# Optimization experiments

Hardware: AMD Instinct MI355X
Metric: run time of the kernel (lower is better)

## Reference

```python
import jax, jax.numpy as jnp
import numpy as np

B, N, S = 8, 16384, 2048
C1, C2 = 128, 256
MLP = [256, 256]
BN_EPS = 1e-5


def setup_inputs() -> dict:
    key = jax.random.key(0)
    ks = jax.random.split(key, 12)
    inp = {
        "xyz1": jax.random.normal(ks[0], (B, N, 3), dtype=jnp.float32),
        "xyz2": jax.random.normal(ks[1], (B, S, 3), dtype=jnp.float32),
        "points1": jax.random.normal(ks[2], (B, C1, N), dtype=jnp.float32),
        "points2": jax.random.normal(ks[3], (B, C2, S), dtype=jnp.float32),
    }
    cin = C1 + C2
    kidx = 4
    for li, cout in enumerate(MLP):
        inp[f"W{li}"] = jax.random.normal(ks[kidx], (cout, cin), dtype=jnp.float32) * (1.0 / np.sqrt(cin))
        inp[f"b{li}"] = jnp.zeros((cout,), dtype=jnp.float32)
        inp[f"g{li}"] = jnp.ones((cout,), dtype=jnp.float32)
        inp[f"beta{li}"] = jnp.zeros((cout,), dtype=jnp.float32)
        cin = cout
        kidx += 1
    return inp


def _interpolate(xyz1, xyz2, points2):
    # D[b,n,s] = ||xyz1[b,n] - xyz2[b,s]||^2
    D = jnp.sum((xyz1[:, :, None, :] - xyz2[:, None, :, :]) ** 2, axis=-1)  # [B,N,S]
    neg_dist, idx = jax.lax.top_k(-D, 3)  # 3 smallest distances, ascending
    dist = jnp.maximum(-neg_dist, 1e-10)  # [B,N,3]
    w = 1.0 / dist
    weight = w / jnp.sum(w, axis=2, keepdims=True)  # [B,N,3]
    p2 = jnp.transpose(points2, (0, 2, 1))  # [B,S,C2]
    gathered = p2[jnp.arange(p2.shape[0])[:, None, None], idx]  # [B,N,3,C2]
    return jnp.einsum("bnkc,bnk->bcn", gathered, weight)  # [B,C2,N]


def _conv_bn_relu(x, W, b, g, beta):
    # 1x1 conv over points: [B,Cin,N] -> [B,Cout,N]
    y = jnp.einsum("oc,bcn->bon", W, x) + b[None, :, None]
    mean = jnp.mean(y, axis=(0, 2), keepdims=True)
    var = jnp.var(y, axis=(0, 2), keepdims=True)  # biased, training-mode BN
    yh = (y - mean) * jax.lax.rsqrt(var + BN_EPS)
    return jax.nn.relu(yh * g[None, :, None] + beta[None, :, None])


def reference(xyz1, xyz2, points1, points2, W0, b0, g0, beta0, W1, b1, g1, beta1):
    interp = _interpolate(xyz1, xyz2, points2)  # [B,C2,N]
    h = jnp.concatenate([interp, points1], axis=1)  # [B,C1+C2,N]
    h = _conv_bn_relu(h, W0, b0, g0, beta0)
    h = _conv_bn_relu(h, W1, b1, g1, beta1)
    return h
```

## Files before the change

### kernel.cpp

```cpp
#include <hip/hip_runtime.h>
#include <hip/hip_bf16.h>


typedef unsigned int u32;
typedef unsigned short u16;
typedef unsigned long long u64;
typedef __attribute__((ext_vector_type(8))) short short8;
typedef __attribute__((ext_vector_type(4))) float f32x4;

#define NT_TOTAL 131072
#define NN 16384
#define SS 2048

__device__ __forceinline__ float bf2f(u16 u) {
    union { u32 i; float f; } cv; cv.i = ((u32)u) << 16; return cv.f;
}
__device__ __forceinline__ u16 f2bf(float f) {
    union { float f; u32 i; } cv; cv.f = f;
    const u32 r = (cv.i + 0x7FFFu + ((cv.i >> 16) & 1u)) >> 16;
    return (u16)r;
}
__device__ __forceinline__ float ldf(const void* p, int i, int isbf) {
    return isbf ? bf2f(((const u16*)p)[i]) : ((const float*)p)[i];
}

__global__ __launch_bounds__(256)
void detect_kernel(const u32* __restrict__ xyz1w, u32* __restrict__ flag,
                   float* __restrict__ stats)
{
    __shared__ int cnt;
    const int t = threadIdx.x;
    if (t == 0) cnt = 0;
    for (int i = t; i < 1024; i += 256) stats[i] = 0.f;
    __syncthreads();
    if (t < 64) {
        const u32 w = xyz1w[t];
        const int e = (int)((w >> 7) & 0xFF);
        if (e >= 96 && e <= 144) atomicAdd(&cnt, 1);
    }
    __syncthreads();
    if (t == 0) flag[0] = (cnt >= 48) ? 1u : 0u;
}

__global__ __launch_bounds__(256)
void sentinel_kernel(u16* __restrict__ out, int n)
{
    const int i = blockIdx.x * 256 + threadIdx.x;
    if (i < n) out[i] = 0x4496;
}

__global__ __launch_bounds__(256)
void param_kernel(const void* W0, const void* b0, const void* g0, const void* bt0,
                  const void* W1, const void* b1, const void* g1, const void* bt1,
                  const u32* __restrict__ flag,
                  u16* __restrict__ Wb0, u16* __restrict__ Wb1, float* __restrict__ pf)
{
    const int isbf = (int)flag[0];
    const int i = blockIdx.x * 256 + threadIdx.x;
    if (i < 98304) Wb0[i] = f2bf(ldf(W0, i, isbf));
    if (i < 65536) Wb1[i] = f2bf(ldf(W1, i, isbf));
    if (i < 1536) {
        const void* srcs[6] = { b0, g0, bt0, b1, g1, bt1 };
        pf[i] = ldf(srcs[i >> 8], i & 255, isbf);
    }
}

__global__ __launch_bounds__(256)
void pack2_kernel(const void* __restrict__ xyz2, float4* __restrict__ s2q,
                  const u32* __restrict__ flag)
{
    const int isbf = (int)flag[0];
    const int i = blockIdx.x * 256 + threadIdx.x;
    if (i < 8 * SS) {
        const float x = ldf(xyz2, i * 3 + 0, isbf);
        const float y = ldf(xyz2, i * 3 + 1, isbf);
        const float z = ldf(xyz2, i * 3 + 2, isbf);
        float4 v; v.x = x; v.y = y; v.z = z; v.w = x * x + y * y + z * z;
        s2q[i] = v;
    }
}

__global__ __launch_bounds__(256)
void transpose_kernel(const void* __restrict__ in, u16* __restrict__ out,
                      int Cc, int Np, int ldout, int coff, const u32* __restrict__ flag)
{
    __shared__ u16 tile[64][72];
    const int isbf = (int)flag[0];
    const int t = threadIdx.x;
    const int n0 = blockIdx.x * 64, c0 = blockIdx.y * 64, bz = blockIdx.z;
    const int ch = t & 7, r = t >> 3;
#pragma unroll
    for (int p = 0; p < 2; ++p) {
        const int cl = r + p * 32;
        const size_t idx = ((size_t)(bz * Cc + c0 + cl)) * Np + n0 + ch * 8;
        union { uint4 v; u16 us[8]; } pk;
        if (isbf) {
            pk.v = *(const uint4*)((const u16*)in + idx);
        } else {
            const float4 va = *(const float4*)((const float*)in + idx);
            const float4 vb = *(const float4*)((const float*)in + idx + 4);
            pk.us[0] = f2bf(va.x); pk.us[1] = f2bf(va.y);
            pk.us[2] = f2bf(va.z); pk.us[3] = f2bf(va.w);
            pk.us[4] = f2bf(vb.x); pk.us[5] = f2bf(vb.y);
            pk.us[6] = f2bf(vb.z); pk.us[7] = f2bf(vb.w);
        }
        *(uint4*)&tile[cl][ch * 8] = pk.v;
    }
    __syncthreads();
#pragma unroll
    for (int p = 0; p < 2; ++p) {
        const int nl = r + p * 32;
        union { uint4 v; u16 us[8]; } pk;
#pragma unroll
        for (int i = 0; i < 8; ++i) pk.us[i] = tile[ch * 8 + i][nl];
        *(uint4*)&out[((size_t)(bz * Np + n0 + nl)) * ldout + coff + c0 + ch * 8] = pk.v;
    }
}

__global__ __launch_bounds__(256)
void knn_kernel(const float4* __restrict__ s2q, const void* __restrict__ xyz1,
                u32* __restrict__ idxA, float* __restrict__ wA,
                const u32* __restrict__ flag)
{
    __shared__ float skeys[4][64][5];
    const int isbf = (int)flag[0];
    const int t = threadIdx.x;
    const int lane = t & 63;
    const int wid = __builtin_amdgcn_readfirstlane(t >> 6);
    const int qg = blockIdx.x * 64 + lane;
    const int b = blockIdx.x >> 8;
    const float qx = ldf(xyz1, qg * 3 + 0, isbf);
    const float qy = ldf(xyz1, qg * 3 + 1, isbf);
    const float qz = ldf(xyz1, qg * 3 + 2, isbf);
    const float qx2 = -2.f * qx, qy2 = -2.f * qy, qz2 = -2.f * qz;
    const float qc = qx * qx + qy * qy + qz * qz;
    const float4* __restrict__ S = s2q + (size_t)b * SS;

    float k0 = __builtin_inff(), k1 = k0, k2 = k0, k3 = k0, k4 = k0;
    const int sbase = wid * 512;
#pragma unroll 8
    for (int it = 0; it < 512; ++it) {
        const int s = sbase + it;
        const float4 v = S[s];
        float d = fmaf(v.x, qx2, qc);
        d = fmaf(v.y, qy2, d);
        d = fmaf(v.z, qz2, d);
        d += v.w;
        const float k = __uint_as_float((__float_as_uint(d) & 0xFFFFF800u) | (u32)s);
        const float o0 = fminf(k, k0);
        const float o1 = __builtin_amdgcn_fmed3f(k, k0, k1);
        const float o2 = __builtin_amdgcn_fmed3f(k, k1, k2);
        const float o3 = __builtin_amdgcn_fmed3f(k, k2, k3);
        const float o4 = __builtin_amdgcn_fmed3f(k, k3, k4);
        k0 = o0; k1 = o1; k2 = o2; k3 = o3; k4 = o4;
    }
    skeys[wid][lane][0] = k0;
    skeys[wid][lane][1] = k1;
    skeys[wid][lane][2] = k2;
    skeys[wid][lane][3] = k3;
    skeys[wid][lane][4] = k4;
    __syncthreads();
    if (wid != 0) return;

    u64 e0 = ~0ull, e1 = ~0ull, e2 = ~0ull;
#pragma unroll
    for (int w = 0; w < 4; ++w)
#pragma unroll
        for (int i = 0; i < 5; ++i) {
            const u32 idx = __float_as_uint(skeys[w][lane][i]) & 0x7FFu;
            const float4 c = S[idx];
            const float dx = qx - c.x, dy = qy - c.y, dz = qz - c.z;
            const float d = fmaf(dz, dz, fmaf(dy, dy, dx * dx));
            const u64 e = ((u64)__float_as_uint(d) << 11) | (u64)idx;
            const bool c0 = e < e0, c1 = e < e1, c2 = e < e2;
            e2 = c1 ? e1 : (c2 ? e : e2);
            e1 = c0 ? e0 : (c1 ? e : e1);
            e0 = c0 ? e : e0;
        }
    const u32 i0 = (u32)(e0 & 0x7FF), i1 = (u32)(e1 & 0x7FF), i2 = (u32)(e2 & 0x7FF);
    const float d0 = fmaxf(__uint_as_float((u32)(e0 >> 11)), 1e-10f);
    const float d1 = fmaxf(__uint_as_float((u32)(e1 >> 11)), 1e-10f);
    const float d2 = fmaxf(__uint_as_float((u32)(e2 >> 11)), 1e-10f);
    const float w0 = 1.f / d0, w1 = 1.f / d1, w2 = 1.f / d2;
    const float inv = 1.f / (w0 + w1 + w2);
    idxA[qg * 3 + 0] = i0; idxA[qg * 3 + 1] = i1; idxA[qg * 3 + 2] = i2;
    wA[qg * 3 + 0] = w0 * inv; wA[qg * 3 + 1] = w1 * inv; wA[qg * 3 + 2] = w2 * inv;
}

__global__ __launch_bounds__(256)
void interp_kernel(const u16* __restrict__ p2T, const u32* __restrict__ idxA,
                   const float* __restrict__ wA, u16* __restrict__ hT)
{
    const int t = threadIdx.x;
    const int pl = t >> 5, g = t & 31;
    const int qg = blockIdx.x * 8 + pl;
    const int b = qg >> 14;
    float acc[8] = {0.f, 0.f, 0.f, 0.f, 0.f, 0.f, 0.f, 0.f};
#pragma unroll
    for (int k = 0; k < 3; ++k) {
        const u32 idx = idxA[qg * 3 + k];
        const float w = wA[qg * 3 + k];
        union { uint4 v; u16 us[8]; } pk;
        pk.v = *(const uint4*)(p2T + ((size_t)(b * SS + idx)) * 256 + g * 8);
#pragma unroll
        for (int e = 0; e < 8; ++e) acc[e] = fmaf(w, bf2f(pk.us[e]), acc[e]);
    }
    union { uint4 v; u16 us[8]; } ov;
#pragma unroll
    for (int e = 0; e < 8; ++e) ov.us[e] = f2bf(acc[e]);
    *(uint4*)&hT[(size_t)qg * 384 + g * 8] = ov.v;
}

__global__ __launch_bounds__(256)
void gemm_kernel(const u16* __restrict__ A, const u16* __restrict__ Bm,
                 const float* __restrict__ bias, void* __restrict__ yout, int K,
                 const u32* __restrict__ flag,
                 float* __restrict__ sums, float* __restrict__ sumsq)
{
    __shared__ __align__(16) u16 aT[128 * 32];
    __shared__ __align__(16) u16 bT[128 * 32];
    const int isbf = (int)flag[0];
    const int t = threadIdx.x;
    const int lane = t & 63;
    const int l15 = lane & 15;
    const int q = lane >> 4;
    const int wid = t >> 6;
    const int n0 = blockIdx.x * 128;
    const int m0 = blockIdx.y * 128;
    const int wm = (wid & 1) * 64;
    const int wn = (wid >> 1) * 64;

    f32x4 acc[4][4] = {};

    const int ca0 = t, ca1 = t + 256;
    const u16* gA0 = A + (size_t)(m0 + (ca0 >> 2)) * K + (ca0 & 3) * 8;
    const u16* gA1 = A + (size_t)(m0 + (ca1 >> 2)) * K + (ca1 & 3) * 8;
    const u16* gB0 = Bm + (size_t)(n0 + (ca0 >> 2)) * K + (ca0 & 3) * 8;
    const u16* gB1 = Bm + (size_t)(n0 + (ca1 >> 2)) * K + (ca1 & 3) * 8;
    u16* lA0 = &aT[ca0 * 8]; u16* lA1 = &aT[ca1 * 8];
    u16* lB0 = &bT[ca0 * 8]; u16* lB1 = &bT[ca1 * 8];

    for (int k0 = 0; k0 < K; k0 += 32) {
        const uint4 ra0 = *(const uint4*)(gA0 + k0);
        const uint4 ra1 = *(const uint4*)(gA1 + k0);
        const uint4 rb0 = *(const uint4*)(gB0 + k0);
        const uint4 rb1 = *(const uint4*)(gB1 + k0);
        __syncthreads();
        *(uint4*)lA0 = ra0; *(uint4*)lA1 = ra1;
        *(uint4*)lB0 = rb0; *(uint4*)lB1 = rb1;
        __syncthreads();
        short8 a[4], b[4];
#pragma unroll
        for (int i = 0; i < 4; ++i)
            a[i] = *(const short8*)&aT[(wm + i * 16 + l15) * 32 + q * 8];
#pragma unroll
        for (int j = 0; j < 4; ++j)
            b[j] = *(const short8*)&bT[(wn + j * 16 + l15) * 32 + q * 8];
#pragma unroll
        for (int i = 0; i < 4; ++i)
#pragma unroll
            for (int j = 0; j < 4; ++j)
                acc[i][j] = __builtin_amdgcn_mfma_f32_16x16x32_bf16(a[i], b[j], acc[i][j], 0, 0, 0);
    }

    __syncthreads();
    float* sdsS = (float*)aT;
    float* sdsQ = (float*)bT;
    if (t < 128) { sdsS[t] = 0.f; sdsQ[t] = 0.f; }
    __syncthreads();
#pragma unroll
    for (int i = 0; i < 4; ++i) {
        const int mloc = wm + i * 16 + q * 4;
#pragma unroll
        for (int r = 0; r < 4; ++r) {
            const float bi = bias[m0 + mloc + r];
            float s = 0.f, sq = 0.f;
#pragma unroll
            for (int j = 0; j < 4; ++j) {
                const float v = acc[i][j][r] + bi;
                s += v; sq += v * v;
            }
#pragma unroll
            for (int off = 1; off < 16; off <<= 1) {
                s += __shfl_xor(s, off);
                sq += __shfl_xor(sq, off);
            }
            if (l15 == 0) {
                atomicAdd(&sdsS[mloc + r], s);
                atomicAdd(&sdsQ[mloc + r], sq);
            }
        }
    }
    __syncthreads();
    if (t < 128) {
        atomicAdd(&sums[m0 + t], sdsS[t]);
        atomicAdd(&sumsq[m0 + t], sdsQ[t]);
    }

#pragma unroll
    for (int i = 0; i < 4; ++i) {
        const int mBase = m0 + wm + i * 16 + q * 4;
        float bi[4];
#pragma unroll
        for (int r = 0; r < 4; ++r) bi[r] = bias[mBase + r];
#pragma unroll
        for (int j = 0; j < 4; ++j) {
            const int col = n0 + wn + j * 16 + l15;
            const size_t obase = ((size_t)(col >> 14) * 256) * NN + (col & 16383);
#pragma unroll
            for (int r = 0; r < 4; ++r) {
                const float v = acc[i][j][r] + bi[r];
                const size_t oi = obase + (size_t)(mBase + r) * NN;
                if (isbf) ((u16*)yout)[oi] = f2bf(v);
                else      ((float*)yout)[oi] = v;
            }
        }
    }
}

__global__ __launch_bounds__(256)
void bn_act_tr_kernel(const void* __restrict__ y, const float* __restrict__ sums,
                      const float* __restrict__ sumsq, const float* __restrict__ gam,
                      const float* __restrict__ beta, u16* __restrict__ h2,
                      const u32* __restrict__ flag)
{
    __shared__ u16 tile[64][68];
    const int isbf = (int)flag[0];
    const int t = threadIdx.x;
    const int n0g = blockIdx.x * 64, c0 = blockIdx.y * 64;
    const int bb = n0g >> 14, nn0 = n0g & 16383;
    const float invNT = 1.0f / (float)NT_TOTAL;
    {
        const int f4 = t & 15, cbase = t >> 4;
#pragma unroll
        for (int p = 0; p < 4; ++p) {
            const int cl = cbase + p * 16;
            const int c = c0 + cl;
            const float mean = sums[c] * invNT;
            const float var = sumsq[c] * invNT - mean * mean;
            const float rstd = rsqrtf(var + 1e-5f);
            const float sc = gam[c] * rstd;
            const float sh = beta[c] - mean * sc;
            const size_t base = ((size_t)(bb * 256 + c)) * NN + nn0 + f4 * 4;
            float in4[4];
            if (isbf) {
                union { uint2 v2; u16 us[4]; } iv;
                iv.v2 = *(const uint2*)((const u16*)y + base);
#pragma unroll
                for (int e = 0; e < 4; ++e) in4[e] = bf2f(iv.us[e]);
            } else {
                const float4 v = *(const float4*)((const float*)y + base);
                in4[0] = v.x; in4[1] = v.y; in4[2] = v.z; in4[3] = v.w;
            }
            union { uint2 v2; u16 us[4]; } o;
#pragma unroll
            for (int e = 0; e < 4; ++e) {
                float v = in4[e] * sc + sh;
                v = (v != v) ? 777.0f : fmaxf(v, 0.f);
                o.us[e] = f2bf(v);
            }
            *(uint2*)&tile[cl][f4 * 4] = o.v2;
        }
    }
    __syncthreads();
    {
        const int ch = t & 7, rr = t >> 3;
#pragma unroll
        for (int p = 0; p < 2; ++p) {
            const int nl = rr + p * 32;
            union { uint4 v; u16 us[8]; } pk;
#pragma unroll
            for (int i = 0; i < 8; ++i) pk.us[i] = tile[ch * 8 + i][nl];
            *(uint4*)&h2[((size_t)(n0g + nl)) * 256 + c0 + ch * 8] = pk.v;
        }
    }
}

__global__ __launch_bounds__(256)
void final_kernel(void* __restrict__ y, const float* __restrict__ sums,
                  const float* __restrict__ sumsq, const float* __restrict__ gam,
                  const float* __restrict__ beta, const u32* __restrict__ flag)
{
    const int isbf = (int)flag[0];
    const int gid = blockIdx.x * 256 + threadIdx.x;
    const int c = (gid >> 12) & 255;
    const float invNT = 1.0f / (float)NT_TOTAL;
    const float mean = sums[c] * invNT;
    const float var = sumsq[c] * invNT - mean * mean;
    const float rstd = rsqrtf(var + 1e-5f);
    const float sc = gam[c] * rstd;
    const float sh = beta[c] - mean * sc;
    const size_t idx4 = (size_t)gid * 4;
    float in4[4];
    if (isbf) {
        union { uint2 v2; u16 us[4]; } iv;
        iv.v2 = *(const uint2*)((const u16*)y + idx4);
#pragma unroll
        for (int e = 0; e < 4; ++e) in4[e] = bf2f(iv.us[e]);
    } else {
        const float4 v = *(const float4*)((const float*)y + idx4);
        in4[0] = v.x; in4[1] = v.y; in4[2] = v.z; in4[3] = v.w;
    }
    float o4[4];
#pragma unroll
    for (int e = 0; e < 4; ++e) {
        float v = in4[e] * sc + sh;
        o4[e] = (v != v) ? 777.0f : fmaxf(v, 0.f);
    }
    if (isbf) {
        union { uint2 v2; u16 us[4]; } o;
#pragma unroll
        for (int e = 0; e < 4; ++e) o.us[e] = f2bf(o4[e]);
        *(uint2*)((u16*)y + idx4) = o.v2;
    } else {
        float4 o; o.x = o4[0]; o.y = o4[1]; o.z = o4[2]; o.w = o4[3];
        *(float4*)((float*)y + idx4) = o;
    }
}

__global__ void pointnet_fp_module_24532853195517_kernel() {}

extern "C" void kernel_launch(void* const* d_in, const int* in_sizes, int n_in,
                              void* d_out, int out_size, void* d_ws, size_t ws_size,
                              hipStream_t stream)
{
    const void* xyz1    = d_in[0];
    const void* xyz2    = d_in[1];
    const void* points1 = d_in[2];
    const void* points2 = d_in[3];
    const void* W0 = d_in[4];  const void* b0 = d_in[5];
    const void* g0 = d_in[6];  const void* bt0 = d_in[7];
    const void* W1 = d_in[8];  const void* b1 = d_in[9];
    const void* g1 = d_in[10]; const void* bt1 = d_in[11];

    char* ws = (char*)d_ws;
    float* stats = (float*)ws;
    u32* flag    = (u32*)(ws + 4096);
    float* pf    = (float*)(ws + 8192);
    u16* Wb0     = (u16*)(ws + 16384);
    u16* Wb1     = (u16*)(ws + 212992);
    u32* idxA    = (u32*)(ws + 344064);
    float* wA    = (float*)(ws + 1916928);
    u16* p2T     = (u16*)(ws + 3489792);
    u16* hT      = (u16*)(ws + 11878400);
    u16* h2      = hT;
    float* sum0 = stats, *sq0 = stats + 256, *sum1 = stats + 512, *sq1 = stats + 768;

    float4* s2q = (float4*)((char*)d_out + (8u << 20));

    if (ws_size < (size_t)112541696) {
        sentinel_kernel<<<(out_size + 255) / 256, 256, 0, stream>>>((u16*)d_out, out_size);
        return;
    }

    sentinel_kernel<<<16, 256, 0, stream>>>((u16*)d_out, 4096);

    detect_kernel<<<1, 256, 0, stream>>>((const u32*)xyz1, flag, stats);
    param_kernel<<<384, 256, 0, stream>>>(W0, b0, g0, bt0, W1, b1, g1, bt1, flag, Wb0, Wb1, pf);
    pack2_kernel<<<64, 256, 0, stream>>>(xyz2, s2q, flag);
    transpose_kernel<<<dim3(32, 4, 8), 256, 0, stream>>>(points2, p2T, 256, 2048, 256, 0, flag);
    transpose_kernel<<<dim3(256, 2, 8), 256, 0, stream>>>(points1, hT, 128, 16384, 384, 256, flag);
    knn_kernel<<<2048, 256, 0, stream>>>(s2q, xyz1, idxA, wA, flag);
    interp_kernel<<<16384, 256, 0, stream>>>(p2T, idxA, wA, hT);
    gemm_kernel<<<dim3(1024, 2), 256, 0, stream>>>(Wb0, hT, pf + 0, d_out, 384, flag, sum0, sq0);
    bn_act_tr_kernel<<<dim3(2048, 4), 256, 0, stream>>>(d_out, sum0, sq0, pf + 256, pf + 512, h2, flag);
    gemm_kernel<<<dim3(1024, 2), 256, 0, stream>>>(Wb1, h2, pf + 768, d_out, 256, flag, sum1, sq1);
    final_kernel<<<32768, 256, 0, stream>>>(d_out, sum1, sq1, pf + 1024, pf + 1280, flag);
}
```

Baseline: 545.2 us.

## Double-buffer GEMM LDS tiles with register prefetch and XOR swizzle

After: 550.0 us. Within noise of the previous version (+0.9%).

```diff
diff --git a/kernel.cpp b/kernel.cpp
--- a/kernel.cpp
+++ b/kernel.cpp
@@ -211,14 +211,39 @@
     *(uint4*)&hT[(size_t)qg * 384 + g * 8] = ov.v;
 }
 
+#define GEMM_BODY(BUF, OTH, KCUR)                                                        \
+    {                                                                                    \
+        short8 a[4], b[4];                                                               \
+        _Pragma("unroll")                                                                \
+        for (int i = 0; i < 4; ++i) a[i] = *(const short8*)&aT[BUF][aoff[i]];            \
+        _Pragma("unroll")                                                                \
+        for (int j = 0; j < 4; ++j) b[j] = *(const short8*)&bT[BUF][boff[j]];            \
+        _Pragma("unroll")                                                                \
+        for (int i = 0; i < 4; ++i)                                                      \
+            _Pragma("unroll")                                                            \
+            for (int j = 0; j < 4; ++j)                                                  \
+                acc[i][j] = __builtin_amdgcn_mfma_f32_16x16x32_bf16(a[i], b[j], acc[i][j], 0, 0, 0); \
+        if ((KCUR) + 32 < K) {                                                           \
+            *(uint4*)&aT[OTH][o0] = ra0; *(uint4*)&aT[OTH][o1] = ra1;                    \
+            *(uint4*)&bT[OTH][o0] = rb0; *(uint4*)&bT[OTH][o1] = rb1;                    \
+            if ((KCUR) + 64 < K) {                                                       \
+                ra0 = *(const uint4*)(gA0 + (KCUR) + 64);                                \
+                ra1 = *(const uint4*)(gA1 + (KCUR) + 64);                                \
+                rb0 = *(const uint4*)(gB0 + (KCUR) + 64);                                \
+                rb1 = *(const uint4*)(gB1 + (KCUR) + 64);                                \
+            }                                                                            \
+        }                                                                                \
+        __syncthreads();                                                                 \
+    }
+
 __global__ __launch_bounds__(256)
 void gemm_kernel(const u16* __restrict__ A, const u16* __restrict__ Bm,
                  const float* __restrict__ bias, void* __restrict__ yout, int K,
                  const u32* __restrict__ flag,
                  float* __restrict__ sums, float* __restrict__ sumsq)
 {
-    __shared__ __align__(16) u16 aT[128 * 32];
-    __shared__ __align__(16) u16 bT[128 * 32];
+    __shared__ __align__(16) u16 aT[2][128 * 32];
+    __shared__ __align__(16) u16 bT[2][128 * 32];
     const int isbf = (int)flag[0];
     const int t = threadIdx.x;
     const int lane = t & 63;
@@ -237,64 +262,32 @@
     const u16* gA1 = A + (size_t)(m0 + (ca1 >> 2)) * K + (ca1 & 3) * 8;
     const u16* gB0 = Bm + (size_t)(n0 + (ca0 >> 2)) * K + (ca0 & 3) * 8;
     const u16* gB1 = Bm + (size_t)(n0 + (ca1 >> 2)) * K + (ca1 & 3) * 8;
-    u16* lA0 = &aT[ca0 * 8]; u16* lA1 = &aT[ca1 * 8];
-    u16* lB0 = &bT[ca0 * 8]; u16* lB1 = &bT[ca1 * 8];
-
-    for (int k0 = 0; k0 < K; k0 += 32) {
-        const uint4 ra0 = *(const uint4*)(gA0 + k0);
-        const uint4 ra1 = *(const uint4*)(gA1 + k0);
-        const uint4 rb0 = *(const uint4*)(gB0 + k0);
-        const uint4 rb1 = *(const uint4*)(gB1 + k0);
-        __syncthreads();
-        *(uint4*)lA0 = ra0; *(uint4*)lA1 = ra1;
-        *(uint4*)lB0 = rb0; *(uint4*)lB1 = rb1;
-        __syncthreads();
-        short8 a[4], b[4];
-#pragma unroll
-        for (int i = 0; i < 4; ++i)
-            a[i] = *(const short8*)&aT[(wm + i * 16 + l15) * 32 + q * 8];
-#pragma unroll
-        for (int j = 0; j < 4; ++j)
-            b[j] = *(const short8*)&bT[(wn + j * 16 + l15) * 32 + q * 8];
-#pragma unroll
-        for (int i = 0; i < 4; ++i)
-#pragma unroll
-            for (int j = 0; j < 4; ++j)
-                acc[i][j] = __builtin_amdgcn_mfma_f32_16x16x32_bf16(a[i], b[j], acc[i][j], 0, 0, 0);
-    }
-
-    __syncthreads();
-    float* sdsS = (float*)aT;
-    float* sdsQ = (float*)bT;
-    if (t < 128) { sdsS[t] = 0.f; sdsQ[t] = 0.f; }
-    __syncthreads();
+    const int o0 = (ca0 >> 2) * 32 + (((ca0 & 3) ^ ((ca0 >> 3) & 3)) * 8);
+    const int o1 = (ca1 >> 2) * 32 + (((ca1 & 3) ^ ((ca1 >> 3) & 3)) * 8);
+
+    const int gsw = (l15 >> 1) & 3;
+    int aoff[4], boff[4];
 #pragma unroll
     for (int i = 0; i < 4; ++i) {
-        const int mloc = wm + i * 16 + q * 4;
-#pragma unroll
-        for (int r = 0; r < 4; ++r) {
-            const float bi = bias[m0 + mloc + r];
-            float s = 0.f, sq = 0.f;
-#pragma unroll
-            for (int j = 0; j < 4; ++j) {
-                const float v = acc[i][j][r] + bi;
-                s += v; sq += v * v;
-            }
-#pragma unroll
-            for (int off = 1; off < 16; off <<= 1) {
-                s += __shfl_xor(s, off);
-                sq += __shfl_xor(sq, off);
-            }
-            if (l15 == 0) {
-                atomicAdd(&sdsS[mloc + r], s);
-                atomicAdd(&sdsQ[mloc + r], sq);
-            }
-        }
-    }
-    __syncthreads();
-    if (t < 128) {
-        atomicAdd(&sums[m0 + t], sdsS[t]);
-        atomicAdd(&sumsq[m0 + t], sdsQ[t]);
+        aoff[i] = (wm + i * 16 + l15) * 32 + ((q ^ gsw) * 8);
+        boff[i] = (wn + i * 16 + l15) * 32 + ((q ^ gsw) * 8);
+    }
+
+    uint4 ra0 = *(const uint4*)(gA0);
+    uint4 ra1 = *(const uint4*)(gA1);
+    uint4 rb0 = *(const uint4*)(gB0);
+    uint4 rb1 = *(const uint4*)(gB1);
+    *(uint4*)&aT[0][o0] = ra0; *(uint4*)&aT[0][o1] = ra1;
+    *(uint4*)&bT[0][o0] = rb0; *(uint4*)&bT[0][o1] = rb1;
+    ra0 = *(const uint4*)(gA0 + 32);
+    ra1 = *(const uint4*)(gA1 + 32);
+    rb0 = *(const uint4*)(gB0 + 32);
+    rb1 = *(const uint4*)(gB1 + 32);
+    __syncthreads();
+
+    for (int kk = 0; kk < K; kk += 64) {
+        GEMM_BODY(0, 1, kk)
+        GEMM_BODY(1, 0, kk + 32)
     }
 
 #pragma unroll
@@ -315,6 +308,39 @@
                 else      ((float*)yout)[oi] = v;
             }
         }
+    }
+
+    float* sds = (float*)&aT[0][0];
+    const int wp = wid >> 1;
+#pragma unroll
+    for (int i = 0; i < 4; ++i) {
+        const int mloc = wm + i * 16 + q * 4;
+#pragma unroll
+        for (int r = 0; r < 4; ++r) {
+            const float bi = bias[m0 + mloc + r];
+            float s = 0.f, sq = 0.f;
+#pragma unroll
+            for (int j = 0; j < 4; ++j) {
+                const float v = acc[i][j][r] + bi;
+                s += v; sq += v * v;
+            }
+#pragma unroll
+            for (int off = 1; off < 16; off <<= 1) {
+                s += __shfl_xor(s, off);
+                sq += __shfl_xor(sq, off);
+            }
+            if (l15 == 0) {
+                sds[wp * 128 + mloc + r] = s;
+                sds[256 + wp * 128 + mloc + r] = sq;
+            }
+        }
+    }
+    __syncthreads();
+    if (t < 128) {
+        atomicAdd(&sums[m0 + t], sds[t] + sds[128 + t]);
+    } else if (t < 256) {
+        const int c = t - 128;
+        atomicAdd(&sumsq[m0 + c], sds[256 + c] + sds[384 + c]);
     }
 }
 
```

## Restructure MLP GEMMs with async LDS loads, in-place layout, sharded BN stats

Applied to the files above, without the earlier changes.

Result: faster. 501.0 us (-8.1%).

```diff
diff --git a/kernel.cpp b/kernel.cpp
--- a/kernel.cpp
+++ b/kernel.cpp
@@ -22,6 +22,15 @@
 }
 __device__ __forceinline__ float ldf(const void* p, int i, int isbf) {
     return isbf ? bf2f(((const u16*)p)[i]) : ((const float*)p)[i];
+}
+
+__device__ __forceinline__ void gll16(const u16* g, const u16* l)
+{
+    typedef __attribute__((address_space(1))) const void gv;
+    typedef __attribute__((address_space(3))) void sv;
+    __builtin_amdgcn_global_load_lds((gv*)(unsigned long long)(const void*)g,
+                                     (sv*)(unsigned int)(unsigned long long)(const void*)l,
+                                     16, 0, 0);
 }
 
 __global__ __launch_bounds__(256)
@@ -78,6 +87,28 @@
         float4 v; v.x = x; v.y = y; v.z = z; v.w = x * x + y * y + z * z;
         s2q[i] = v;
     }
+}
+
+__global__ __launch_bounds__(256)
+void zero_kernel(float* __restrict__ a, float* __restrict__ b)
+{
+    const int i = blockIdx.x * 256 + threadIdx.x;
+    if (i < 32768) { a[i] = 0.f; b[i] = 0.f; }
+}
+
+__global__ __launch_bounds__(256)
+void reduce_kernel(const float* __restrict__ sh, float* __restrict__ outSum,
+                   float* __restrict__ outSq)
+{
+    const int t = threadIdx.x;
+    float s = 0.f, q = 0.f;
+#pragma unroll 8
+    for (int j = 0; j < 64; ++j) {
+        s += sh[j * 512 + t];
+        q += sh[j * 512 + 256 + t];
+    }
+    outSum[t] = s;
+    outSq[t] = q;
 }
 
 __global__ __launch_bounds__(256)
@@ -211,14 +242,133 @@
     *(uint4*)&hT[(size_t)qg * 384 + g * 8] = ov.v;
 }
 
-__global__ __launch_bounds__(256)
-void gemm_kernel(const u16* __restrict__ A, const u16* __restrict__ Bm,
-                 const float* __restrict__ bias, void* __restrict__ yout, int K,
-                 const u32* __restrict__ flag,
-                 float* __restrict__ sums, float* __restrict__ sumsq)
-{
-    __shared__ __align__(16) u16 aT[128 * 32];
-    __shared__ __align__(16) u16 bT[128 * 32];
+#define K0 384
+__global__ __launch_bounds__(256)
+void gemm0_kernel(const u16* __restrict__ A, u16* __restrict__ hTio,
+                  const float* __restrict__ bias, float* __restrict__ sh0)
+{
+    __shared__ __align__(16) u16 aB[2][256 * 32];
+    __shared__ __align__(16) u16 bB[2][64 * 32];
+    __shared__ float sds[512];
+    const int t = threadIdx.x;
+    const int lane = t & 63;
+    const int l15 = lane & 15;
+    const int q = lane >> 4;
+    const int wid = t >> 6;
+    const int n0 = blockIdx.x * 64;
+    const int wm = wid * 64;
+
+    f32x4 acc[4][4] = {};
+
+    const u16* gB = hTio + (size_t)(n0 + (t >> 2)) * 384 + (t & 3) * 8;
+    const u16* gA = A + (size_t)(t >> 2) * K0 + (t & 3) * 8;
+
+    gll16(gB, &bB[0][t * 8]);
+#pragma unroll
+    for (int p = 0; p < 4; ++p)
+        gll16(gA + (size_t)p * 64 * K0, &aB[0][(p * 256 + t) * 8]);
+    __syncthreads();
+
+#pragma unroll
+    for (int kk = 0; kk < K0; kk += 32) {
+        const int cur = (kk >> 5) & 1;
+        if (kk + 32 < K0) {
+            gll16(gB + kk + 32, &bB[cur ^ 1][t * 8]);
+#pragma unroll
+            for (int p = 0; p < 4; ++p)
+                gll16(gA + (size_t)p * 64 * K0 + kk + 32, &aB[cur ^ 1][(p * 256 + t) * 8]);
+        }
+        short8 a4[4], b4[4];
+#pragma unroll
+        for (int i = 0; i < 4; ++i)
+            a4[i] = *(const short8*)&aB[cur][(wm + i * 16 + l15) * 32 + q * 8];
+#pragma unroll
+        for (int j = 0; j < 4; ++j)
+            b4[j] = *(const short8*)&bB[cur][(j * 16 + l15) * 32 + q * 8];
+#pragma unroll
+        for (int i = 0; i < 4; ++i)
+#pragma unroll
+            for (int j = 0; j < 4; ++j)
+                acc[i][j] = __builtin_amdgcn_mfma_f32_16x16x32_bf16(a4[i], b4[j], acc[i][j], 0, 0, 0);
+        __syncthreads();
+    }
+
+#pragma unroll
+    for (int i = 0; i < 4; ++i) {
+        const int mcb = wm + i * 16 + q * 4;
+        float bi4[4];
+#pragma unroll
+        for (int r = 0; r < 4; ++r) bi4[r] = bias[mcb + r];
+#pragma unroll
+        for (int j = 0; j < 4; ++j) {
+            const int nl = j * 16 + l15;
+            union { u64 w; u16 us[4]; } pk;
+#pragma unroll
+            for (int r = 0; r < 4; ++r) pk.us[r] = f2bf(acc[i][j][r] + bi4[r]);
+            *(u64*)&hTio[(size_t)(n0 + nl) * 384 + mcb] = pk.w;
+        }
+#pragma unroll
+        for (int r = 0; r < 4; ++r) {
+            float s = 0.f, sq = 0.f;
+#pragma unroll
+            for (int j = 0; j < 4; ++j) {
+                const float v = acc[i][j][r] + bi4[r];
+                s += v; sq += v * v;
+            }
+#pragma unroll
+            for (int off = 1; off < 16; off <<= 1) {
+                s += __shfl_xor(s, off);
+                sq += __shfl_xor(sq, off);
+            }
+            if (l15 == 0) { sds[mcb + r] = s; sds[256 + mcb + r] = sq; }
+        }
+    }
+    __syncthreads();
+    const int jsh = blockIdx.x & 63;
+    atomicAdd(&sh0[jsh * 512 + t], sds[t]);
+    atomicAdd(&sh0[jsh * 512 + 256 + t], sds[256 + t]);
+}
+
+__global__ __launch_bounds__(256)
+void bn_kernel(u16* __restrict__ hT, const float* __restrict__ sums,
+               const float* __restrict__ sumsq, const float* __restrict__ gam,
+               const float* __restrict__ beta)
+{
+    __shared__ float ssc[256], ssh[256];
+    const int t = threadIdx.x;
+    {
+        const float invNT = 1.0f / (float)NT_TOTAL;
+        const float mean = sums[t] * invNT;
+        const float var = sumsq[t] * invNT - mean * mean;
+        const float rstd = rsqrtf(var + 1e-5f);
+        const float sc = gam[t] * rstd;
+        ssc[t] = sc;
+        ssh[t] = beta[t] - mean * sc;
+    }
+    __syncthreads();
+    const int row = blockIdx.x * 8 + (t >> 5);
+    const int cb = (t & 31) * 8;
+    u16* p = hT + (size_t)row * 384 + cb;
+    union { uint4 v; u16 us[8]; } pk;
+    pk.v = *(const uint4*)p;
+#pragma unroll
+    for (int e = 0; e < 8; ++e) {
+        float v = bf2f(pk.us[e]) * ssc[cb + e] + ssh[cb + e];
+        v = (v != v) ? 777.0f : fmaxf(v, 0.f);
+        pk.us[e] = f2bf(v);
+    }
+    *(uint4*)p = pk.v;
+}
+
+#define K1 256
+__global__ __launch_bounds__(256)
+void gemm1_kernel(const u16* __restrict__ A, const u16* __restrict__ h2,
+                  const float* __restrict__ bias, void* __restrict__ yout,
+                  const u32* __restrict__ flag, float* __restrict__ sh1)
+{
+    __shared__ __align__(16) u16 aB[2][128 * 32];
+    __shared__ __align__(16) u16 bB[2][128 * 32];
+    __shared__ float sds[512];
     const int isbf = (int)flag[0];
     const int t = threadIdx.x;
     const int lane = t & 63;
@@ -229,72 +379,43 @@
     const int m0 = blockIdx.y * 128;
     const int wm = (wid & 1) * 64;
     const int wn = (wid >> 1) * 64;
+    const int wp = wid >> 1;
 
     f32x4 acc[4][4] = {};
 
-    const int ca0 = t, ca1 = t + 256;
-    const u16* gA0 = A + (size_t)(m0 + (ca0 >> 2)) * K + (ca0 & 3) * 8;
-    const u16* gA1 = A + (size_t)(m0 + (ca1 >> 2)) * K + (ca1 & 3) * 8;
-    const u16* gB0 = Bm + (size_t)(n0 + (ca0 >> 2)) * K + (ca0 & 3) * 8;
-    const u16* gB1 = Bm + (size_t)(n0 + (ca1 >> 2)) * K + (ca1 & 3) * 8;
-    u16* lA0 = &aT[ca0 * 8]; u16* lA1 = &aT[ca1 * 8];
-    u16* lB0 = &bT[ca0 * 8]; u16* lB1 = &bT[ca1 * 8];
-
-    for (int k0 = 0; k0 < K; k0 += 32) {
-        const uint4 ra0 = *(const uint4*)(gA0 + k0);
-        const uint4 ra1 = *(const uint4*)(gA1 + k0);
-        const uint4 rb0 = *(const uint4*)(gB0 + k0);
-        const uint4 rb1 = *(const uint4*)(gB1 + k0);
+    const u16* gB0 = h2 + (size_t)(n0 + (t >> 2)) * 384 + (t & 3) * 8;
+    const u16* gB1 = gB0 + (size_t)64 * 384;
+    const u16* gA0 = A + (size_t)(m0 + (t >> 2)) * K1 + (t & 3) * 8;
+    const u16* gA1 = gA0 + (size_t)64 * K1;
+
+    gll16(gA0, &aB[0][t * 8]);
+    gll16(gA1, &aB[0][(256 + t) * 8]);
+    gll16(gB0, &bB[0][t * 8]);
+    gll16(gB1, &bB[0][(256 + t) * 8]);
+    __syncthreads();
+
+#pragma unroll
+    for (int kk = 0; kk < K1; kk += 32) {
+        const int cur = (kk >> 5) & 1;
+        if (kk + 32 < K1) {
+            gll16(gA0 + kk + 32, &aB[cur ^ 1][t * 8]);
+            gll16(gA1 + kk + 32, &aB[cur ^ 1][(256 + t) * 8]);
+            gll16(gB0 + kk + 32, &bB[cur ^ 1][t * 8]);
+            gll16(gB1 + kk + 32, &bB[cur ^ 1][(256 + t) * 8]);
+        }
+        short8 a4[4], b4[4];
+#pragma unroll
+        for (int i = 0; i < 4; ++i)
+            a4[i] = *(const short8*)&aB[cur][(wm + i * 16 + l15) * 32 + q * 8];
+#pragma unroll
+        for (int j = 0; j < 4; ++j)
+            b4[j] = *(const short8*)&bB[cur][(wn + j * 16 + l15) * 32 + q * 8];
+#pragma unroll
+        for (int i = 0; i < 4; ++i)
+#pragma unroll
+            for (int j = 0; j < 4; ++j)
+                acc[i][j] = __builtin_amdgcn_mfma_f32_16x16x32_bf16(a4[i], b4[j], acc[i][j], 0, 0, 0);
         __syncthreads();
-        *(uint4*)lA0 = ra0; *(uint4*)lA1 = ra1;
-        *(uint4*)lB0 = rb0; *(uint4*)lB1 = rb1;
-        __syncthreads();
-        short8 a[4], b[4];
-#pragma unroll
-        for (int i = 0; i < 4; ++i)
-            a[i] = *(const short8*)&aT[(wm + i * 16 + l15) * 32 + q * 8];
-#pragma unroll
-        for (int j = 0; j < 4; ++j)
-            b[j] = *(const short8*)&bT[(wn + j * 16 + l15) * 32 + q * 8];
-#pragma unroll
-        for (int i = 0; i < 4; ++i)
-#pragma unroll
-            for (int j = 0; j < 4; ++j)
-                acc[i][j] = __builtin_amdgcn_mfma_f32_16x16x32_bf16(a[i], b[j], acc[i][j], 0, 0, 0);
-    }
-
-    __syncthreads();
-    float* sdsS = (float*)aT;
-    float* sdsQ = (float*)bT;
-    if (t < 128) { sdsS[t] = 0.f; sdsQ[t] = 0.f; }
-    __syncthreads();
-#pragma unroll
-    for (int i = 0; i < 4; ++i) {
-        const int mloc = wm + i * 16 + q * 4;
-#pragma unroll
-        for (int r = 0; r < 4; ++r) {
-            const float bi = bias[m0 + mloc + r];
-            float s = 0.f, sq = 0.f;
-#pragma unroll
-            for (int j = 0; j < 4; ++j) {
-                const float v = acc[i][j][r] + bi;
-                s += v; sq += v * v;
-            }
-#pragma unroll
-            for (int off = 1; off < 16; off <<= 1) {
-                s += __shfl_xor(s, off);
-                sq += __shfl_xor(sq, off);
-            }
-            if (l15 == 0) {
-                atomicAdd(&sdsS[mloc + r], s);
-                atomicAdd(&sdsQ[mloc + r], sq);
-            }
-        }
-    }
-    __syncthreads();
-    if (t < 128) {
-        atomicAdd(&sums[m0 + t], sdsS[t]);
-        atomicAdd(&sumsq[m0 + t], sdsQ[t]);
     }
 
 #pragma unroll
@@ -316,63 +437,36 @@
             }
         }
     }
-}
-
-__global__ __launch_bounds__(256)
-void bn_act_tr_kernel(const void* __restrict__ y, const float* __restrict__ sums,
-                      const float* __restrict__ sumsq, const float* __restrict__ gam,
-                      const float* __restrict__ beta, u16* __restrict__ h2,
-                      const u32* __restrict__ flag)
-{
-    __shared__ u16 tile[64][68];
-    const int isbf = (int)flag[0];
-    const int t = threadIdx.x;
-    const int n0g = blockIdx.x * 64, c0 = blockIdx.y * 64;
-    const int bb = n0g >> 14, nn0 = n0g & 16383;
-    const float invNT = 1.0f / (float)NT_TOTAL;
-    {
-        const int f4 = t & 15, cbase = t >> 4;
-#pragma unroll
-        for (int p = 0; p < 4; ++p) {
-            const int cl = cbase + p * 16;
-            const int c = c0 + cl;
-            const float mean = sums[c] * invNT;
-            const float var = sumsq[c] * invNT - mean * mean;
-            const float rstd = rsqrtf(var + 1e-5f);
-            const float sc = gam[c] * rstd;
-            const float sh = beta[c] - mean * sc;
-            const size_t base = ((size_t)(bb * 256 + c)) * NN + nn0 + f4 * 4;
-            float in4[4];
-            if (isbf) {
-                union { uint2 v2; u16 us[4]; } iv;
-                iv.v2 = *(const uint2*)((const u16*)y + base);
-#pragma unroll
-                for (int e = 0; e < 4; ++e) in4[e] = bf2f(iv.us[e]);
-            } else {
-                const float4 v = *(const float4*)((const float*)y + base);
-                in4[0] = v.x; in4[1] = v.y; in4[2] = v.z; in4[3] = v.w;
+#pragma unroll
+    for (int i = 0; i < 4; ++i) {
+        const int mloc = wm + i * 16 + q * 4;
+#pragma unroll
+        for (int r = 0; r < 4; ++r) {
+            const float bi = bias[m0 + mloc + r];
+            float s = 0.f, sq = 0.f;
+#pragma unroll
+            for (int j = 0; j < 4; ++j) {
+                const float v = acc[i][j][r] + bi;
+                s += v; sq += v * v;
             }
-            union { uint2 v2; u16 us[4]; } o;
-#pragma unroll
-            for (int e = 0; e < 4; ++e) {
-                float v = in4[e] * sc + sh;
-                v = (v != v) ? 777.0f : fmaxf(v, 0.f);
-                o.us[e] = f2bf(v);
+#pragma unroll
+            for (int off = 1; off < 16; off <<= 1) {
+                s += __shfl_xor(s, off);
+                sq += __shfl_xor(sq, off);
             }
-            *(uint2*)&tile[cl][f4 * 4] = o.v2;
-        }
-    }
-    __syncthreads();
-    {
-        const int ch = t & 7, rr = t >> 3;
-#pragma unroll
-        for (int p = 0; p < 2; ++p) {
-            const int nl = rr + p * 32;
-            union { uint4 v; u16 us[8]; } pk;
-#pragma unroll
-            for (int i = 0; i < 8; ++i) pk.us[i] = tile[ch * 8 + i][nl];
-            *(uint4*)&h2[((size_t)(n0g + nl)) * 256 + c0 + ch * 8] = pk.v;
-        }
+            if (l15 == 0) {
+                sds[wp * 128 + mloc + r] = s;
+                sds[256 + wp * 128 + mloc + r] = sq;
+            }
+        }
+    }
+    __syncthreads();
+    const int jsh = blockIdx.x & 63;
+    if (t < 128) {
+        atomicAdd(&sh1[jsh * 512 + m0 + t], sds[t] + sds[128 + t]);
+    } else if (t < 256) {
+        const int c = t - 128;
+        atomicAdd(&sh1[jsh * 512 + 256 + m0 + c], sds[256 + c] + sds[384 + c]);
     }
 }
 
@@ -443,8 +537,10 @@
     float* wA    = (float*)(ws + 1916928);
     u16* p2T     = (u16*)(ws + 3489792);
     u16* hT      = (u16*)(ws + 11878400);
-    u16* h2      = hT;
     float* sum0 = stats, *sq0 = stats + 256, *sum1 = stats + 512, *sq1 = stats + 768;
+
+    float* sh0 = (float*)p2T;
+    float* sh1 = sh0 + 32768;
 
     float4* s2q = (float4*)((char*)d_out + (8u << 20));
 
@@ -462,8 +558,11 @@
     transpose_kernel<<<dim3(256, 2, 8), 256, 0, stream>>>(points1, hT, 128, 16384, 384, 256, flag);
     knn_kernel<<<2048, 256, 0, stream>>>(s2q, xyz1, idxA, wA, flag);
     interp_kernel<<<16384, 256, 0, stream>>>(p2T, idxA, wA, hT);
-    gemm_kernel<<<dim3(1024, 2), 256, 0, stream>>>(Wb0, hT, pf + 0, d_out, 384, flag, sum0, sq0);
-    bn_act_tr_kernel<<<dim3(2048, 4), 256, 0, stream>>>(d_out, sum0, sq0, pf + 256, pf + 512, h2, flag);
-    gemm_kernel<<<dim3(1024, 2), 256, 0, stream>>>(Wb1, h2, pf + 768, d_out, 256, flag, sum1, sq1);
+    zero_kernel<<<128, 256, 0, stream>>>(sh0, sh1);
+    gemm0_kernel<<<2048, 256, 0, stream>>>(Wb0, hT, pf + 0, sh0);
+    reduce_kernel<<<1, 256, 0, stream>>>(sh0, sum0, sq0);
+    bn_kernel<<<16384, 256, 0, stream>>>(hT, sum0, sq0, pf + 256, pf + 512);
+    gemm1_kernel<<<dim3(1024, 2), 256, 0, stream>>>(Wb1, hT, pf + 768, d_out, flag, sh1);
+    reduce_kernel<<<1, 256, 0, stream>>>(sh1, sum1, sq1);
     final_kernel<<<32768, 256, 0, stream>>>(d_out, sum1, sq1, pf + 1024, pf + 1280, flag);
 }
```
